# Kernel optimization log

Hardware: AMD Instinct MI355X
Metric: run time of the kernel (lower is better)

The kernel has to match this reference:

```python
import jax, jax.numpy as jnp
import numpy as np

B, IN_CH, H, W = 4, 1, 512, 512
DEPTH, WIDTH = 12, 2
DILATIONS = tuple(range(1, DEPTH + 1))


def setup_inputs() -> dict:
    key = jax.random.key(0)
    ks = jax.random.split(key, DEPTH + 2)
    inp = {"x": jax.random.normal(ks[0], (B, IN_CH, H, W), jnp.float32)}
    inp["bias"] = jax.random.normal(ks[1], (DEPTH * WIDTH,), jnp.float32) * 0.01
    for i in range(DEPTH):
        n_in = IN_CH + WIDTH * i
        # kaiming-ish scale for 3x3 kernel with n_in input channels
        inp[f"w{i}"] = jax.random.normal(ks[2 + i], (WIDTH, n_in, 3, 3), jnp.float32) / np.sqrt(9.0 * n_in)
    return inp


def _dilated_conv_relu(x, w, b, d):
    # msd_pytorch's conv2d_relu_forward: reflection-padded dilated 3x3 conv + bias + ReLU,
    # preserving spatial size (pad = dilation).
    xp = jnp.pad(x, ((0, 0), (0, 0), (d, d), (d, d)), mode='reflect')
    y = jax.lax.conv_general_dilated(
        xp, w, window_strides=(1, 1), padding='VALID',
        rhs_dilation=(d, d), dimension_numbers=('NCHW', 'OIHW', 'NCHW'))
    return jax.nn.relu(y + b[None, :, None, None])


def reference(x, bias, w0, w1, w2, w3, w4, w5, w6, w7, w8, w9, w10, w11):
    weights = (w0, w1, w2, w3, w4, w5, w6, w7, w8, w9, w10, w11)
    buf = x  # growing dense buffer: each layer consumes all previous channels
    for i, w in enumerate(weights):
        b = bias[i * WIDTH:(i + 1) * WIDTH]
        y = _dilated_conv_relu(buf, w, b, DILATIONS[i])
        buf = jnp.concatenate([buf, y], axis=1)
    return buf  # (B, IN_CH + DEPTH*WIDTH, H, W)
```

## Files before the change

kernel.cpp:

```cpp
#include <hip/hip_runtime.h>

#define HH 512
#define WW 512
#define NB 4
#define NC 25
#define HWs (HH * WW)

__device__ __forceinline__ int refl(int p, int n) {
    p = (p < 0) ? -p : p;
    p = (p >= n) ? (2 * n - 2 - p) : p;
    return p;
}

__global__ __launch_bounds__(256) void copy_x_kernel(const float* __restrict__ x,
                                                     float* __restrict__ out) {
    int t = blockIdx.x * 256 + threadIdx.x;
    int b = t >> 16;
    int r = t & 65535;
    const float4* src = (const float4*)(x + (size_t)b * HWs);
    float4* dst = (float4*)(out + (size_t)b * NC * HWs);
    dst[r] = src[r];
}

template <int NIN, int DIL>
__global__ __launch_bounds__(256) void msd_layer(const float* __restrict__ wts,
                                                 const float* __restrict__ bias,
                                                 float* __restrict__ buf,
                                                 int layer) {
    constexpr int M3 = 512 / (3 * DIL);
    constexpr int DM = DIL * M3;
    constexpr int SPAN = 3 * DM;
    constexpr int RT = 512 - SPAN;
    constexpr int TCH = (RT + 3) / 4;
    constexpr int IMT = 512 * DM;
    constexpr int NMAIN = 4 * IMT;

    const int t = blockIdx.x * 256 + threadIdx.x;
    const float b0 = bias[2 * layer];
    const float b1 = bias[2 * layer + 1];

    if (t < NMAIN) {
        const int img = t / IMT;
        const int u = t - img * IMT;
        const int bi = __builtin_amdgcn_readfirstlane(u >> 9);
        const int w = u & 511;
        const int k = bi / DIL, j = bi - k * DIL;
        const int h = 3 * DIL * k + j;

        int rowoff[5];
#pragma unroll
        for (int r = 0; r < 5; ++r) rowoff[r] = refl(h + (r - 1) * DIL, HH) * WW;
        int cw[3];
#pragma unroll
        for (int q = 0; q < 3; ++q) cw[q] = refl(w + (q - 1) * DIL, WW);

        float a0[3] = {b0, b0, b0};
        float a1[3] = {b1, b1, b1};
        const float* base = buf + (size_t)img * NC * HWs;

        for (int c = 0; c < NIN; ++c) {
            const float* plane = base + (size_t)c * HWs;
            float v[5][3];
#pragma unroll
            for (int r = 0; r < 5; ++r) {
                const float* rowp = plane + rowoff[r];
#pragma unroll
                for (int q = 0; q < 3; ++q) v[r][q] = rowp[cw[q]];
            }
            float wk0[9], wk1[9];
#pragma unroll
            for (int kk = 0; kk < 9; ++kk) {
                wk0[kk] = wts[c * 9 + kk];
                wk1[kk] = wts[(NIN + c) * 9 + kk];
            }
#pragma unroll
            for (int al = 0; al < 3; ++al)
#pragma unroll
                for (int kr = 0; kr < 3; ++kr)
#pragma unroll
                    for (int kw = 0; kw < 3; ++kw) {
                        float vv = v[al + kr][kw];
                        a0[al] = fmaf(vv, wk0[kr * 3 + kw], a0[al]);
                        a1[al] = fmaf(vv, wk1[kr * 3 + kw], a1[al]);
                    }
        }

        float* o0 = buf + (size_t)(img * NC + NIN) * HWs;
        float* o1 = o0 + HWs;
#pragma unroll
        for (int al = 0; al < 3; ++al) {
            size_t off = (size_t)(h + al * DIL) * WW + (size_t)w;
            o0[off] = fmaxf(a0[al], 0.f);
            o1[off] = fmaxf(a1[al], 0.f);
        }
    } else if (RT > 0) {
        const int t2 = t - NMAIN;
        constexpr int PIT = 512 * TCH;
        const int img = t2 / PIT;
        const int u = t2 - img * PIT;
        const int s = __builtin_amdgcn_readfirstlane(u >> 9);
        const int w = u & 511;
        const int r0 = SPAN + 4 * s;

        int cw[3];
#pragma unroll
        for (int q = 0; q < 3; ++q) cw[q] = refl(w + (q - 1) * DIL, WW);
        int ro[3][4];
#pragma unroll
        for (int kr = 0; kr < 3; ++kr)
#pragma unroll
            for (int i = 0; i < 4; ++i)
                ro[kr][i] = refl(r0 + i + (kr - 1) * DIL, HH) * WW;

        float a0[4] = {b0, b0, b0, b0};
        float a1[4] = {b1, b1, b1, b1};
        const float* base = buf + (size_t)img * NC * HWs;

        for (int c = 0; c < NIN; ++c) {
            const float* plane = base + (size_t)c * HWs;
            float wk0[9], wk1[9];
#pragma unroll
            for (int kk = 0; kk < 9; ++kk) {
                wk0[kk] = wts[c * 9 + kk];
                wk1[kk] = wts[(NIN + c) * 9 + kk];
            }
#pragma unroll
            for (int i = 0; i < 4; ++i) {
                if (r0 + i < HH) {
#pragma unroll
                    for (int kr = 0; kr < 3; ++kr) {
                        const float* rowp = plane + ro[kr][i];
#pragma unroll
                        for (int kw = 0; kw < 3; ++kw) {
                            float vv = rowp[cw[kw]];
                            a0[i] = fmaf(vv, wk0[kr * 3 + kw], a0[i]);
                            a1[i] = fmaf(vv, wk1[kr * 3 + kw], a1[i]);
                        }
                    }
                }
            }
        }

        float* o0 = buf + (size_t)(img * NC + NIN) * HWs;
        float* o1 = o0 + HWs;
#pragma unroll
        for (int i = 0; i < 4; ++i) {
            if (r0 + i < HH) {
                size_t off = (size_t)(r0 + i) * WW + (size_t)w;
                o0[off] = fmaxf(a0[i], 0.f);
                o1[off] = fmaxf(a1[i], 0.f);
            }
        }
    }
}

extern "C" void kernel_launch(void* const* d_in, const int* in_sizes, int n_in,
                              void* d_out, int out_size, void* d_ws, size_t ws_size,
                              hipStream_t stream) {
    const float* x = (const float*)d_in[0];
    const float* bias = (const float*)d_in[1];
    float* out = (float*)d_out;

    copy_x_kernel<<<1024, 256, 0, stream>>>(x, out);

#define GBLK(dil) (8 * ((512 / (3 * (dil))) * (dil)) \
                 + 8 * (((512 - 3 * ((512 / (3 * (dil))) * (dil))) + 3) / 4))
#define LAYER(i, nin, dil) \
    msd_layer<nin, dil><<<GBLK(dil), 256, 0, stream>>>((const float*)d_in[2 + i], bias, out, i)

    LAYER(0, 1, 1);
    LAYER(1, 3, 2);
    LAYER(2, 5, 3);
    LAYER(3, 7, 4);
    LAYER(4, 9, 5);
    LAYER(5, 11, 6);
    LAYER(6, 13, 7);
    LAYER(7, 15, 8);
    LAYER(8, 17, 9);
    LAYER(9, 19, 10);
    LAYER(10, 21, 11);
    LAYER(11, 23, 12);
#undef LAYER
#undef GBLK
}
```

Before: 387.6 us.

## Prefetch next channel's inputs and weights, remap blocks across XCDs, add occupancy hint

```diff
diff --git a/kernel.cpp b/kernel.cpp
--- a/kernel.cpp
+++ b/kernel.cpp
@@ -23,10 +23,10 @@
 }
 
 template <int NIN, int DIL>
-__global__ __launch_bounds__(256) void msd_layer(const float* __restrict__ wts,
-                                                 const float* __restrict__ bias,
-                                                 float* __restrict__ buf,
-                                                 int layer) {
+__global__ __launch_bounds__(256, 4) void msd_layer(const float* __restrict__ wts,
+                                                    const float* __restrict__ bias,
+                                                    float* __restrict__ buf,
+                                                    int layer) {
     constexpr int M3 = 512 / (3 * DIL);
     constexpr int DM = DIL * M3;
     constexpr int SPAN = 3 * DM;
@@ -35,7 +35,15 @@
     constexpr int IMT = 512 * DM;
     constexpr int NMAIN = 4 * IMT;
 
-    const int t = blockIdx.x * 256 + threadIdx.x;
+    int bid = blockIdx.x;
+    {
+        const int nblk = gridDim.x;
+        const int q = nblk >> 3, r = nblk & 7;
+        const int xcd = bid & 7, idx = bid >> 3;
+        bid = (xcd < r ? xcd * (q + 1) : r * (q + 1) + (xcd - r) * q) + idx;
+    }
+    const int t = bid * 256 + threadIdx.x;
+
     const float b0 = bias[2 * layer];
     const float b1 = bias[2 * layer + 1];
 
@@ -58,21 +66,39 @@
         float a1[3] = {b1, b1, b1};
         const float* base = buf + (size_t)img * NC * HWs;
 
+        float v[5][3];
+#pragma unroll
+        for (int r = 0; r < 5; ++r) {
+            const float* rowp = base + rowoff[r];
+#pragma unroll
+            for (int q = 0; q < 3; ++q) v[r][q] = rowp[cw[q]];
+        }
+        float wk0[9], wk1[9];
+#pragma unroll
+        for (int kk = 0; kk < 9; ++kk) {
+            wk0[kk] = wts[kk];
+            wk1[kk] = wts[NIN * 9 + kk];
+        }
+
+#pragma unroll
         for (int c = 0; c < NIN; ++c) {
-            const float* plane = base + (size_t)c * HWs;
-            float v[5][3];
-#pragma unroll
-            for (int r = 0; r < 5; ++r) {
-                const float* rowp = plane + rowoff[r];
-#pragma unroll
-                for (int q = 0; q < 3; ++q) v[r][q] = rowp[cw[q]];
-            }
-            float wk0[9], wk1[9];
-#pragma unroll
-            for (int kk = 0; kk < 9; ++kk) {
-                wk0[kk] = wts[c * 9 + kk];
-                wk1[kk] = wts[(NIN + c) * 9 + kk];
-            }
+            float vn[5][3];
+            float wn0[9], wn1[9];
+            if (c + 1 < NIN) {
+                const float* pn = base + (size_t)(c + 1) * HWs;
+#pragma unroll
+                for (int r = 0; r < 5; ++r) {
+                    const float* rowp = pn + rowoff[r];
+#pragma unroll
+                    for (int q = 0; q < 3; ++q) vn[r][q] = rowp[cw[q]];
+                }
+#pragma unroll
+                for (int kk = 0; kk < 9; ++kk) {
+                    wn0[kk] = wts[(c + 1) * 9 + kk];
+                    wn1[kk] = wts[(NIN + c + 1) * 9 + kk];
+                }
+            }
+
 #pragma unroll
             for (int al = 0; al < 3; ++al)
 #pragma unroll
@@ -83,6 +109,18 @@
                         a0[al] = fmaf(vv, wk0[kr * 3 + kw], a0[al]);
                         a1[al] = fmaf(vv, wk1[kr * 3 + kw], a1[al]);
                     }
+
+            if (c + 1 < NIN) {
+#pragma unroll
+                for (int r = 0; r < 5; ++r)
+#pragma unroll
+                    for (int q = 0; q < 3; ++q) v[r][q] = vn[r][q];
+#pragma unroll
+                for (int kk = 0; kk < 9; ++kk) {
+                    wk0[kk] = wn0[kk];
+                    wk1[kk] = wn1[kk];
+                }
+            }
         }
 
         float* o0 = buf + (size_t)(img * NC + NIN) * HWs;
```

Result: faster. 365.4 us (-5.7%).

## Stage main-path input rows in LDS via async double-buffered global_load_lds

Applied to the files above, without the earlier changes.

```diff
diff --git a/kernel.cpp b/kernel.cpp
--- a/kernel.cpp
+++ b/kernel.cpp
@@ -22,11 +22,17 @@
     dst[r] = src[r];
 }
 
+__device__ __forceinline__ void gload_lds(const float* g, float* l) {
+    __builtin_amdgcn_global_load_lds(
+        (const __attribute__((address_space(1))) void*)g,
+        (__attribute__((address_space(3))) void*)l, 4, 0, 0);
+}
+
 template <int NIN, int DIL>
-__global__ __launch_bounds__(256) void msd_layer(const float* __restrict__ wts,
-                                                 const float* __restrict__ bias,
-                                                 float* __restrict__ buf,
-                                                 int layer) {
+__global__ __launch_bounds__(256, 4) void msd_layer(const float* __restrict__ wts,
+                                                    const float* __restrict__ bias,
+                                                    float* __restrict__ buf,
+                                                    int layer) {
     constexpr int M3 = 512 / (3 * DIL);
     constexpr int DM = DIL * M3;
     constexpr int SPAN = 3 * DM;
@@ -35,7 +41,23 @@
     constexpr int IMT = 512 * DM;
     constexpr int NMAIN = 4 * IMT;
 
-    const int t = blockIdx.x * 256 + threadIdx.x;
+    constexpr int SW = 256 + 2 * DIL;
+    constexpr int TOT = 5 * SW;
+    constexpr int ROUNDS = (TOT + 255) / 256;
+    constexpr int LPAD = ROUNDS * 256;
+
+    __shared__ float smem[2][LPAD];
+
+    int bid = blockIdx.x;
+    {
+        const int nblk = gridDim.x;
+        const int q = nblk >> 3, r = nblk & 7;
+        const int xcd = bid & 7, idx = bid >> 3;
+        bid = (xcd < r ? xcd * (q + 1) : r * (q + 1) + (xcd - r) * q) + idx;
+    }
+    const int t = bid * 256 + threadIdx.x;
+    const int tid = threadIdx.x;
+
     const float b0 = bias[2 * layer];
     const float b1 = bias[2 * layer + 1];
 
@@ -44,35 +66,62 @@
         const int u = t - img * IMT;
         const int bi = __builtin_amdgcn_readfirstlane(u >> 9);
         const int w = u & 511;
+        const int wc = w & 255;
+        const int c0 = w - wc;
         const int k = bi / DIL, j = bi - k * DIL;
         const int h = 3 * DIL * k + j;
 
-        int rowoff[5];
-#pragma unroll
-        for (int r = 0; r < 5; ++r) rowoff[r] = refl(h + (r - 1) * DIL, HH) * WW;
-        int cw[3];
-#pragma unroll
-        for (int q = 0; q < 3; ++q) cw[q] = refl(w + (q - 1) * DIL, WW);
+        int soff[ROUNDS];
+#pragma unroll
+        for (int it = 0; it < ROUNDS; ++it) {
+            int f = it * 256 + tid;
+            int fc = (f < TOT) ? f : (TOT - 1);
+            int r = fc / SW;
+            int jj = fc - r * SW;
+            int row = refl(h + (r - 1) * DIL, HH);
+            int col = refl(c0 - DIL + jj, WW);
+            soff[it] = row * WW + col;
+        }
+        const int wbase = tid & 192;
+
+        const float* base = buf + (size_t)img * NC * HWs;
 
         float a0[3] = {b0, b0, b0};
         float a1[3] = {b1, b1, b1};
-        const float* base = buf + (size_t)img * NC * HWs;
-
+
+        {
+            const float* plane = base;
+#pragma unroll
+            for (int it = 0; it < ROUNDS; ++it)
+                gload_lds(plane + soff[it], &smem[0][it * 256 + wbase]);
+        }
+
+        int cur = 0;
+#pragma unroll
         for (int c = 0; c < NIN; ++c) {
-            const float* plane = base + (size_t)c * HWs;
+            __syncthreads();
+
+            if (c + 1 < NIN) {
+                const float* plane = base + (size_t)(c + 1) * HWs;
+#pragma unroll
+                for (int it = 0; it < ROUNDS; ++it)
+                    gload_lds(plane + soff[it], &smem[cur ^ 1][it * 256 + wbase]);
+            }
+
             float v[5][3];
 #pragma unroll
-            for (int r = 0; r < 5; ++r) {
-                const float* rowp = plane + rowoff[r];
-#pragma unroll
-                for (int q = 0; q < 3; ++q) v[r][q] = rowp[cw[q]];
-            }
+            for (int r = 0; r < 5; ++r)
+#pragma unroll
+                for (int q = 0; q < 3; ++q)
+                    v[r][q] = smem[cur][r * SW + wc + q * DIL];
+
             float wk0[9], wk1[9];
 #pragma unroll
             for (int kk = 0; kk < 9; ++kk) {
                 wk0[kk] = wts[c * 9 + kk];
                 wk1[kk] = wts[(NIN + c) * 9 + kk];
             }
+
 #pragma unroll
             for (int al = 0; al < 3; ++al)
 #pragma unroll
@@ -83,6 +132,8 @@
                         a0[al] = fmaf(vv, wk0[kr * 3 + kw], a0[al]);
                         a1[al] = fmaf(vv, wk1[kr * 3 + kw], a1[al]);
                     }
+
+            cur ^= 1;
         }
 
         float* o0 = buf + (size_t)(img * NC + NIN) * HWs;
```

Result: slower. 453.2 us (+16.9%).

## Remap blocks across XCDs, stagger channel order, and double-buffer channel loads

Applied to the files above, without the earlier changes.

```diff
diff --git a/kernel.cpp b/kernel.cpp
--- a/kernel.cpp
+++ b/kernel.cpp
@@ -2,7 +2,6 @@
 
 #define HH 512
 #define WW 512
-#define NB 4
 #define NC 25
 #define HWs (HH * WW)
 
@@ -23,10 +22,10 @@
 }
 
 template <int NIN, int DIL>
-__global__ __launch_bounds__(256) void msd_layer(const float* __restrict__ wts,
-                                                 const float* __restrict__ bias,
-                                                 float* __restrict__ buf,
-                                                 int layer) {
+__global__ __launch_bounds__(256, 4) void msd_layer(const float* __restrict__ wts,
+                                                    const float* __restrict__ bias,
+                                                    float* __restrict__ buf,
+                                                    int layer) {
     constexpr int M3 = 512 / (3 * DIL);
     constexpr int DM = DIL * M3;
     constexpr int SPAN = 3 * DM;
@@ -35,7 +34,15 @@
     constexpr int IMT = 512 * DM;
     constexpr int NMAIN = 4 * IMT;
 
-    const int t = blockIdx.x * 256 + threadIdx.x;
+    int bid = blockIdx.x;
+    {
+        const int nblk = gridDim.x;
+        const int q = nblk >> 3, r = nblk & 7;
+        const int xcd = bid & 7, idx = bid >> 3;
+        bid = (xcd < r ? xcd * (q + 1) : r * (q + 1) + (xcd - r) * q) + idx;
+    }
+    const int t = bid * 256 + threadIdx.x;
+
     const float b0 = bias[2 * layer];
     const float b1 = bias[2 * layer + 1];
 
@@ -58,15 +65,20 @@
         float a1[3] = {b1, b1, b1};
         const float* base = buf + (size_t)img * NC * HWs;
 
-        for (int c = 0; c < NIN; ++c) {
+        const int c0 = bid - (bid / NIN) * NIN;
+
+        float vA[5][3], vB[5][3];
+
+        auto LD = [&](float (&v)[5][3], int c) {
             const float* plane = base + (size_t)c * HWs;
-            float v[5][3];
 #pragma unroll
             for (int r = 0; r < 5; ++r) {
                 const float* rowp = plane + rowoff[r];
 #pragma unroll
                 for (int q = 0; q < 3; ++q) v[r][q] = rowp[cw[q]];
             }
+        };
+        auto FM = [&](const float (&v)[5][3], int c) {
             float wk0[9], wk1[9];
 #pragma unroll
             for (int kk = 0; kk < 9; ++kk) {
@@ -83,6 +95,19 @@
                         a0[al] = fmaf(vv, wk0[kr * 3 + kw], a0[al]);
                         a1[al] = fmaf(vv, wk1[kr * 3 + kw], a1[al]);
                     }
+        };
+
+        LD(vA, c0);
+#pragma unroll
+        for (int i = 0; i < NIN; i += 2) {
+            int cA = c0 + i;     cA -= (cA >= NIN) ? NIN : 0;
+            int cB = c0 + i + 1; cB -= (cB >= NIN) ? NIN : 0;
+            if (i + 1 < NIN) LD(vB, cB);
+            FM(vA, cA);
+            if (i + 1 >= NIN) break;
+            int cN = c0 + i + 2; cN -= (cN >= NIN) ? NIN : 0;
+            if (i + 2 < NIN) LD(vA, cN);
+            FM(vB, cB);
         }
 
         float* o0 = buf + (size_t)(img * NC + NIN) * HWs;
```

Result: faster. 362.6 us (-6.4%).
